# Performance work log

Hardware: AMD Instinct MI355X
Metric: run time of the kernel (lower is better)

The kernel has to match this reference:

```python
import jax, jax.numpy as jnp
import numpy as np

NS, NV = 16, 4          # scalar / vector multiplicities
MODES = 2               # spectral conv retained fourier modes
C_OUT = 40              # out irreps dim: 16 + 4*3 + 4*3
EPS = 1e-5


def setup_inputs() -> dict:
    key = jax.random.key(0)
    ks = jax.random.split(key, 10)
    T, N, E = 8, 10000, 32768
    x = jax.random.normal(ks[0], (T, N, 28), jnp.float32)
    edge_index = jax.random.randint(ks[1], (2, E), 0, N)
    edge_attr = jax.random.normal(ks[2], (T, E, 48), jnp.float32)
    edge_sh = jax.random.normal(ks[3], (T, E, 4), jnp.float32)
    s = 1.0 / np.sqrt(48.0)
    w_mlp1 = jax.random.normal(ks[4], (48, 48), jnp.float32) * s
    b_mlp1 = jnp.zeros((48,), jnp.float32)
    w_mlp2 = jax.random.normal(ks[5], (48, 416), jnp.float32) * s
    b_mlp2 = jnp.zeros((416,), jnp.float32)
    sc = 1.0 / (NS * NS)
    tc_wr = jax.random.uniform(ks[6], (NS, NS, MODES), jnp.float32) * sc
    tc_wi = jax.random.uniform(ks[7], (NS, NS, MODES), jnp.float32) * sc
    bn_gamma = jnp.ones((C_OUT,), jnp.float32)
    bn_beta = jnp.zeros((C_OUT,), jnp.float32)
    return dict(x=x, edge_index=edge_index, edge_attr=edge_attr, edge_sh=edge_sh,
                w_mlp1=w_mlp1, b_mlp1=b_mlp1, w_mlp2=w_mlp2, b_mlp2=b_mlp2,
                tc_wr=tc_wr, tc_wi=tc_wi, bn_gamma=bn_gamma, bn_beta=bn_beta)


def reference(x, edge_index, edge_attr, edge_sh,
              w_mlp1, b_mlp1, w_mlp2, b_mlp2,
              tc_wr, tc_wi, bn_gamma, bn_beta):
    T, N, _ = x.shape
    E = edge_index.shape[1]
    src, dst = edge_index[0], edge_index[1]

    # ---- SpectralConv1d over the time axis (scalar channels only) ----
    xs = x[:, :, :NS]                                   # [T,N,16]
    xf = jnp.fft.rfft(xs, axis=0)                       # [T//2+1,N,16] c64
    w = tc_wr + 1j * tc_wi                              # [16,16,M]
    low = jnp.einsum('tni,iom->tno', xf[:MODES], jnp.moveaxis(w, -1, 0).transpose(1, 2, 0)[..., :MODES]) if False else jnp.einsum('mni,iom->mno', xf[:MODES], w)
    out_ft = jnp.zeros((T // 2 + 1, N, NS), jnp.complex64).at[:MODES].set(low)
    x_scalar = jnp.fft.irfft(out_ft, n=T, axis=0)       # [T,N,16]

    # ---- edge MLP -> per-edge tensor-product weights [T,E,416] ----
    h = jax.nn.relu(edge_attr @ w_mlp1 + b_mlp1)
    ew = h @ w_mlp2 + b_mlp2

    # ---- gather source node features per edge ----
    xe = x[:, src]                                      # [T,E,28]
    s = xe[..., :NS]                                    # [T,E,16]
    v = xe[..., NS:].reshape(T, E, NV, 3)               # [T,E,4,3]
    sh0 = edge_sh[..., :1]                              # [T,E,1]
    sh1 = edge_sh[..., 1:4]                             # [T,E,3]

    # path weight splits: 0e*0e->0e | 0e*1o->1o | 1o*0e->1o | 1o*1o->0e | 1o*1o->1e
    w00 = ew[..., 0:256].reshape(T, E, NS, NS)
    w01 = ew[..., 256:320].reshape(T, E, NS, NV)
    w10 = ew[..., 320:336].reshape(T, E, NV, NV)
    w110 = ew[..., 336:400].reshape(T, E, NV, NS)
    w111 = ew[..., 400:416].reshape(T, E, NV, NV)

    inv3 = 1.0 / np.sqrt(3.0)
    inv6 = 1.0 / np.sqrt(6.0)
    n0 = 1.0 / np.sqrt(20.0)   # fan-in norm for 0e output (16 + 4 paths)
    n1o = 1.0 / np.sqrt(20.0)  # fan-in norm for 1o output (16 + 4 paths)
    n1e = 1.0 / np.sqrt(4.0)   # fan-in norm for 1e output

    # scalar outputs
    p1 = jnp.einsum('tei,teio->teo', s * sh0, w00)
    vdots = jnp.einsum('teid,ted->tei', v, sh1) * inv3
    p4 = jnp.einsum('tei,teio->teo', vdots, w110)
    out0 = (p1 + p4) * n0                               # [T,E,16]

    # odd-vector outputs
    p2 = jnp.einsum('tei,teio->teo', s, w01)[..., None] * sh1[:, :, None, :] * inv3
    p3 = jnp.einsum('teid,teio->teod', v * sh0[..., None], w10) * inv3
    out1o = (p2 + p3) * n1o                             # [T,E,4,3]

    c = jnp.cross(v, sh1[:, :, None, :]) * inv6
    out1e = jnp.einsum('teid,teio->teod', c, w111) * n1e  # [T,E,4,3]

    msg = jnp.concatenate([out0,
                           out1o.reshape(T, E, NV * 3),
                           out1e.reshape(T, E, NV * 3)], axis=-1)  # [T,E,40]

    # ---- scatter_mean over destination nodes ----
    seg = jax.vmap(lambda m: jax.ops.segment_sum(m, dst, num_segments=N))(msg)
    cnt = jax.ops.segment_sum(jnp.ones((E,), msg.dtype), dst, num_segments=N)
    y = seg / jnp.maximum(cnt, 1.0)[None, :, None]      # [T,N,40]

    # ---- add spectral time-conv result to scalar channels ----
    y = jnp.concatenate([y[..., :NS] + x_scalar, y[..., NS:]], axis=-1)

    # ---- BatchNorm1d replicating torch permute/reshape semantics ----
    z = jnp.transpose(y, (1, 2, 0)).reshape(-1, C_OUT)  # [N*T, 40] (torch layout)
    mu = z.mean(axis=0)
    var = z.var(axis=0)
    z = (z - mu) / jnp.sqrt(var + EPS) * bn_gamma + bn_beta
    y = jnp.transpose(z.reshape(N, C_OUT, T), (2, 0, 1))
    return y
```

## Files before the change

### kernel.cpp

```cpp
#include <hip/hip_runtime.h>
#include <math.h>

#define TT 8
#define NN 10000
#define EE 32768
#define CC 40
#define EPSV 1e-05f

constexpr float INV3 = 0.57735026918962576f;
constexpr float INV6 = 0.40824829046386302f;
constexpr float N0F  = 0.22360679774997896f;
constexpr float N1OF = 0.22360679774997896f;
constexpr float N1EF = 0.5f;

constexpr float CTab[8] = {1.f, 0.70710678118654752f, 0.f, -0.70710678118654752f,
                           -1.f, -0.70710678118654752f, 0.f, 0.70710678118654752f};
constexpr float STab[8] = {0.f, 0.70710678118654752f, 1.f, 0.70710678118654752f,
                           0.f, -0.70710678118654752f, -1.f, -0.70710678118654752f};

typedef __attribute__((ext_vector_type(8))) short short8;
typedef __attribute__((ext_vector_type(4))) float f32x4;

__device__ __forceinline__ void atomAdd(float* p, float v) {
  __hip_atomic_fetch_add(p, v, __ATOMIC_RELAXED, __HIP_MEMORY_SCOPE_AGENT);
}

__device__ __forceinline__ short f2bfs(float f) {
  unsigned u = __builtin_bit_cast(unsigned, f);
  u = (u + 0x7fffu + ((u >> 16) & 1u)) >> 16;
  return (short)u;
}
__device__ __forceinline__ float bf2f(ushort u) {
  unsigned v = ((unsigned)u) << 16;
  return __builtin_bit_cast(float, v);
}

#define SPEC_B 157
#define DEG_B  128
#define PREP_B 116
__global__ __launch_bounds__(256) void k_pre(const float* __restrict__ x,
                                             const float* __restrict__ wr,
                                             const float* __restrict__ wi,
                                             const int* __restrict__ ei,
                                             const float* __restrict__ W1,
                                             const float* __restrict__ W2,
                                             float* __restrict__ xsc,
                                             int* __restrict__ deg,
                                             short* __restrict__ W1F,
                                             short* __restrict__ W2F) {
  int b = blockIdx.x, tid = threadIdx.x;
  if (b < SPEC_B) {
    int gid = b * 256 + tid;
    int n = gid >> 2, og = gid & 3;
    if (n >= NN) return;
    float F0[16], A[16], B[16];
#pragma unroll
    for (int i = 0; i < 16; ++i) { F0[i] = 0.f; A[i] = 0.f; B[i] = 0.f; }
#pragma unroll
    for (int t = 0; t < 8; ++t) {
      const float4* xp = (const float4*)(x + ((size_t)t * NN + n) * 28);
      float4 v0 = xp[0], v1 = xp[1], v2 = xp[2], v3 = xp[3];
      const float ct = CTab[t], st = STab[t];
      float vv[16] = {v0.x, v0.y, v0.z, v0.w, v1.x, v1.y, v1.z, v1.w,
                      v2.x, v2.y, v2.z, v2.w, v3.x, v3.y, v3.z, v3.w};
#pragma unroll
      for (int i = 0; i < 16; ++i) {
        F0[i] += vv[i];
        A[i] = fmaf(vv[i], ct, A[i]);
        B[i] = fmaf(vv[i], -st, B[i]);
      }
    }
#pragma unroll
    for (int oo = 0; oo < 4; ++oo) {
      int o = og * 4 + oo;
      float r0 = 0.f, r1 = 0.f, i1 = 0.f;
#pragma unroll
      for (int i = 0; i < 16; ++i) {
        float wr0 = wr[i * 32 + o * 2 + 0];
        float wr1 = wr[i * 32 + o * 2 + 1];
        float wi1 = wi[i * 32 + o * 2 + 1];
        r0 = fmaf(F0[i], wr0, r0);
        r1 += A[i] * wr1 - B[i] * wi1;
        i1 += A[i] * wi1 + B[i] * wr1;
      }
#pragma unroll
      for (int t = 0; t < 8; ++t) {
        float val = 0.125f * (r0 + 2.f * (r1 * CTab[t] - i1 * STab[t]));
        xsc[((size_t)t * NN + n) * 16 + o] = val;
      }
    }
  } else if (b < SPEC_B + DEG_B) {
    int e = (b - SPEC_B) * 256 + tid;
    if (e < EE) atomicAdd(&deg[ei[EE + e]], 1);
  } else {
    int idx = (b - SPEC_B - DEG_B) * 256 + tid;
    const int tot1 = 3 * 2 * 64 * 8;
    if (idx < tot1) {
      int elem = idx & 7, lane = (idx >> 3) & 63, kt = (idx >> 9) & 1, nt = idx >> 10;
      int j = kt * 32 + ((lane >> 4) << 2) + (elem & 3) + ((elem >> 2) << 4);
      int n = nt * 16 + (lane & 15);
      W1F[idx] = (j < 48) ? f2bfs(W1[j * 48 + n]) : (short)0;
    } else {
      int id2 = idx - tot1;
      int elem = id2 & 7, lane = (id2 >> 3) & 63, kt = (id2 >> 9) & 1, ck = id2 >> 10;
      int j = kt * 32 + ((lane >> 4) << 2) + (elem & 3) + ((elem >> 2) << 4);
      int n = ck * 16 + (lane & 15);
      W2F[id2] = (j < 48) ? f2bfs(W2[j * 416 + n]) : (short)0;
    }
  }
}

__global__ __launch_bounds__(1024) void k_scan(const int* __restrict__ deg,
                                               int* __restrict__ row_start,
                                               int* __restrict__ cursor,
                                               float* __restrict__ stats) {
  __shared__ int sums[1024];
  int tid = threadIdx.x;
  if (tid < 80) stats[tid] = 0.f;
  const int PER = 10;
  int base = tid * PER;
  int s = 0;
#pragma unroll
  for (int i = 0; i < PER; ++i) {
    int idx = base + i;
    if (idx < NN) s += deg[idx];
  }
  sums[tid] = s;
  __syncthreads();
  for (int off = 1; off < 1024; off <<= 1) {
    int add = (tid >= off) ? sums[tid - off] : 0;
    __syncthreads();
    sums[tid] += add;
    __syncthreads();
  }
  int run = sums[tid] - s;
#pragma unroll
  for (int i = 0; i < PER; ++i) {
    int idx = base + i;
    if (idx < NN) {
      row_start[idx] = run;
      cursor[idx] = run;
      run += deg[idx];
    }
  }
  if (tid == 1023) row_start[NN] = run;
}

__global__ __launch_bounds__(256) void k_bucket(const int* __restrict__ ei,
                                                int* __restrict__ cursor,
                                                int* __restrict__ ipos) {
  int e = blockIdx.x * 256 + threadIdx.x;
  if (e >= EE) return;
  int d = ei[EE + e];
  int slot = atomicAdd(&cursor[d], 1);
  ipos[e] = slot;
}

__global__ __launch_bounds__(256, 4) void k_edge4(
    const float* __restrict__ x,
    const int* __restrict__ ei,
    const float* __restrict__ eag,
    const float* __restrict__ shg,
    const short* __restrict__ W1F,
    const short* __restrict__ W2F,
    const float* __restrict__ b1,
    const float* __restrict__ b2,
    const int* __restrict__ ipos,
    ushort* __restrict__ msg)
{
  __shared__ float cSs[16][64];
  __shared__ float rawSs[16][64];
  __shared__ float cVDs[4][64];
  __shared__ float vS0s[12][64];
  __shared__ float sh1fs[3][64];
  __shared__ float cCRs[12][64];
  __shared__ int   iposs[64];
  __shared__ ushort Hs[4][16][64];

  int blk = blockIdx.x;
  int t = blk >> 9;
  int e0 = (blk & 511) * 64;
  int tid = threadIdx.x;

  {
    int e = tid & 63;
    int role = tid >> 6;
    int eg = e0 + e;
    const float* shp = shg + ((size_t)t * EE + eg) * 4;
    float sh0 = shp[0], s1x = shp[1], s1y = shp[2], s1z = shp[3];
    int src = ei[eg];
    const float* xr = x + ((size_t)t * NN + src) * 28;
    const float F1 = INV3 * N1OF;
    if (role == 0) {
      iposs[e] = ipos[eg];
      sh1fs[0][e] = s1x * F1; sh1fs[1][e] = s1y * F1; sh1fs[2][e] = s1z * F1;
#pragma unroll
      for (int i = 0; i < 8; ++i) {
        float s = xr[i];
        rawSs[i][e] = s;
        cSs[i][e] = s * sh0 * N0F;
      }
    } else if (role == 1) {
#pragma unroll
      for (int i = 8; i < 16; ++i) {
        float s = xr[i];
        rawSs[i][e] = s;
        cSs[i][e] = s * sh0 * N0F;
      }
    } else {
      int i0 = (role == 2) ? 0 : 2;
#pragma unroll
      for (int ii = 0; ii < 2; ++ii) {
        int i = i0 + ii;
        float vx = xr[16 + 3 * i], vy = xr[17 + 3 * i], vz = xr[18 + 3 * i];
        cVDs[i][e] = (vx * s1x + vy * s1y + vz * s1z) * INV3 * N0F;
        vS0s[3 * i + 0][e] = vx * sh0 * F1;
        vS0s[3 * i + 1][e] = vy * sh0 * F1;
        vS0s[3 * i + 2][e] = vz * sh0 * F1;
        cCRs[3 * i + 0][e] = (vy * s1z - vz * s1y) * INV6 * N1EF;
        cCRs[3 * i + 1][e] = (vz * s1x - vx * s1z) * INV6 * N1EF;
        cCRs[3 * i + 2][e] = (vx * s1y - vy * s1x) * INV6 * N1EF;
      }
    }
  }
  __syncthreads();

  int w = tid >> 6, l = tid & 63;
  int col = l & 15;
  int kq  = (l >> 4) << 2;
  int eb  = w * 16;

  const float* row = eag + ((size_t)t * EE + e0 + eb + col) * 48;
  float4 fa = *(const float4*)(row + kq);
  float4 fb = *(const float4*)(row + 16 + kq);
  float4 fc = *(const float4*)(row + 32 + kq);
  short8 a0, a1;
  a0[0] = f2bfs(fa.x); a0[1] = f2bfs(fa.y); a0[2] = f2bfs(fa.z); a0[3] = f2bfs(fa.w);
  a0[4] = f2bfs(fb.x); a0[5] = f2bfs(fb.y); a0[6] = f2bfs(fb.z); a0[7] = f2bfs(fb.w);
  a1[0] = f2bfs(fc.x); a1[1] = f2bfs(fc.y); a1[2] = f2bfs(fc.z); a1[3] = f2bfs(fc.w);
  a1[4] = 0; a1[5] = 0; a1[6] = 0; a1[7] = 0;

  const short8* w1f = (const short8*)W1F;
  const short8* w2f = (const short8*)W2F;

#pragma unroll
  for (int nt = 0; nt < 3; ++nt) {
    float bias = b1[nt * 16 + col];
    f32x4 c = {bias, bias, bias, bias};
    c = __builtin_amdgcn_mfma_f32_16x16x32_bf16(a0, w1f[(nt * 2 + 0) * 64 + l], c, 0, 0, 0);
    c = __builtin_amdgcn_mfma_f32_16x16x32_bf16(a1, w1f[(nt * 2 + 1) * 64 + l], c, 0, 0, 0);
#pragma unroll
    for (int r = 0; r < 4; ++r) {
      int m = kq + r;
      float hv = fmaxf(c[r], 0.f);
      Hs[w][m][(nt * 16 + col) ^ ((m & 7) << 3)] = (ushort)f2bfs(hv);
    }
  }
#pragma unroll
  for (int r = 0; r < 4; ++r) {
    int m = kq + r;
    Hs[w][m][(48 + col) ^ ((m & 7) << 3)] = 0;
  }

  int m2 = col, X = (m2 & 7) << 3;
  ushort4 r0 = *(const ushort4*)&Hs[w][m2][(kq +  0) ^ X];
  ushort4 r1 = *(const ushort4*)&Hs[w][m2][(kq + 16) ^ X];
  ushort4 r2 = *(const ushort4*)&Hs[w][m2][(kq + 32) ^ X];
  ushort4 r3 = *(const ushort4*)&Hs[w][m2][(kq + 48) ^ X];
  short8 A20, A21;
  A20[0] = (short)r0.x; A20[1] = (short)r0.y; A20[2] = (short)r0.z; A20[3] = (short)r0.w;
  A20[4] = (short)r1.x; A20[5] = (short)r1.y; A20[6] = (short)r1.z; A20[7] = (short)r1.w;
  A21[0] = (short)r2.x; A21[1] = (short)r2.y; A21[2] = (short)r2.z; A21[3] = (short)r2.w;
  A21[4] = (short)r3.x; A21[5] = (short)r3.y; A21[6] = (short)r3.z; A21[7] = (short)r3.w;

  float acc0[4]  = {0.f, 0.f, 0.f, 0.f};
  float accP2[4] = {0.f, 0.f, 0.f, 0.f};
  float acc1o[3][4] = {{0.f,0.f,0.f,0.f},{0.f,0.f,0.f,0.f},{0.f,0.f,0.f,0.f}};
  float acc1e[3][4] = {{0.f,0.f,0.f,0.f},{0.f,0.f,0.f,0.f},{0.f,0.f,0.f,0.f}};
  int er0 = eb + kq;
  int iloc = col >> 2;
  int o = col & 3;

  short8 pf0[4], pf1[4];
#pragma unroll
  for (int i = 0; i < 4; ++i) {
    pf0[i] = w2f[(2 * i + 0) * 64 + l];
    pf1[i] = w2f[(2 * i + 1) * 64 + l];
  }

#pragma unroll
  for (int ck = 0; ck < 26; ++ck) {
    short8 B0 = pf0[ck & 3], B1 = pf1[ck & 3];
    if (ck + 4 < 26) {
      pf0[ck & 3] = w2f[(2 * (ck + 4) + 0) * 64 + l];
      pf1[ck & 3] = w2f[(2 * (ck + 4) + 1) * 64 + l];
    }
    float bias = b2[ck * 16 + col];
    f32x4 c = {bias, bias, bias, bias};
    c = __builtin_amdgcn_mfma_f32_16x16x32_bf16(A20, B0, c, 0, 0, 0);
    c = __builtin_amdgcn_mfma_f32_16x16x32_bf16(A21, B1, c, 0, 0, 0);

    if (ck < 16) {
#pragma unroll
      for (int r = 0; r < 4; ++r)
        acc0[r] = fmaf(cSs[ck][er0 + r], c[r], acc0[r]);
    } else if (ck < 20) {
#pragma unroll
      for (int r = 0; r < 4; ++r) {
        float q = rawSs[(ck - 16) * 4 + iloc][er0 + r] * c[r];
        q += __shfl_xor(q, 4);
        q += __shfl_xor(q, 8);
        accP2[r] += q;
      }
    } else if (ck == 20) {
#pragma unroll
      for (int d = 0; d < 3; ++d)
#pragma unroll
        for (int r = 0; r < 4; ++r) {
          float q = vS0s[iloc * 3 + d][er0 + r] * c[r];
          q += __shfl_xor(q, 4);
          q += __shfl_xor(q, 8);
          acc1o[d][r] += q;
        }
    } else if (ck < 25) {
#pragma unroll
      for (int r = 0; r < 4; ++r)
        acc0[r] = fmaf(cVDs[ck - 21][er0 + r], c[r], acc0[r]);
    } else {
#pragma unroll
      for (int d = 0; d < 3; ++d)
#pragma unroll
        for (int r = 0; r < 4; ++r) {
          float q = cCRs[iloc * 3 + d][er0 + r] * c[r];
          q += __shfl_xor(q, 4);
          q += __shfl_xor(q, 8);
          acc1e[d][r] += q;
        }
    }
  }

#pragma unroll
  for (int r = 0; r < 4; ++r) {
    size_t eg = (size_t)t * EE + iposs[er0 + r];
    msg[eg * 40 + col] = (ushort)f2bfs(acc0[r]);
  }
  if (col < 4) {
#pragma unroll
    for (int r = 0; r < 4; ++r) {
      int e = er0 + r;
      size_t eg = (size_t)t * EE + iposs[e];
      ushort* mrow = msg + eg * 40;
#pragma unroll
      for (int d = 0; d < 3; ++d) {
        mrow[16 + 3 * o + d] = (ushort)f2bfs(fmaf(accP2[r], sh1fs[d][e], acc1o[d][r]));
        mrow[28 + 3 * o + d] = (ushort)f2bfs(acc1e[d][r]);
      }
    }
  }
}

__global__ __launch_bounds__(320) void k_gstats(const ushort* __restrict__ msg,
                                                const int* __restrict__ row_start,
                                                const float* __restrict__ xsc,
                                                float* __restrict__ out,
                                                float* __restrict__ stats) {
  int blk = blockIdx.x;
  int t = blk / 157;
  int nb = blk - t * 157;
  int tid = threadIdx.x;
  int g = tid / 40, c = tid - g * 40;
  int r5 = c % 5;
  __shared__ float sred[10];
  if (tid < 10) sred[tid] = 0.f;
  __syncthreads();
  float p = 0.f, q = 0.f;
  for (int step = 0; step < 8; ++step) {
    int n = nb * 64 + step * 8 + g;
    if (n < NN) {
      int a = row_start[n], b = row_start[n + 1];
      float acc = 0.f;
      for (int j = a; j < b; ++j)
        acc += bf2f(msg[((size_t)t * EE + j) * 40 + c]);
      float y = acc / fmaxf((float)(b - a), 1.f) +
                (c < 16 ? xsc[((size_t)t * NN + n) * 16 + c] : 0.f);
      out[((size_t)t * NN + n) * 40 + c] = y;
      p += y;
      q = fmaf(y, y, q);
    }
  }
  atomicAdd(&sred[r5], p);
  atomicAdd(&sred[5 + r5], q);
  __syncthreads();
  if (tid < 10) {
    int r = tid % 5;
    int j = 8 * r + t;
    atomAdd(stats + (tid >= 5 ? 40 + j : j), sred[tid]);
  }
}

__global__ __launch_bounds__(256) void k_norm(const float* __restrict__ stats,
                                              const float* __restrict__ gam,
                                              const float* __restrict__ bet,
                                              float* __restrict__ out) {
  int idx4 = blockIdx.x * 256 + threadIdx.x;
  if (idx4 >= TT * NN * 10) return;
  int t = idx4 / (NN * 10);
  int rem = idx4 - t * NN * 10;
  int c0 = (rem % 10) * 4;
  const float inv = 1.f / (8.f * (float)NN);
  float4* op = (float4*)out;
  float4 y = op[idx4];
  float vals[4] = {y.x, y.y, y.z, y.w};
#pragma unroll
  for (int k = 0; k < 4; ++k) {
    int c = c0 + k;
    int j = 8 * (c % 5) + t;
    float mu = stats[j] * inv;
    float var = stats[40 + j] * inv - mu * mu;
    vals[k] = (vals[k] - mu) * rsqrtf(var + EPSV) * gam[j] + bet[j];
  }
  y.x = vals[0]; y.y = vals[1]; y.z = vals[2]; y.w = vals[3];
  op[idx4] = y;
}

extern "C" void kernel_launch(void* const* d_in, const int* in_sizes, int n_in,
                              void* d_out, int out_size, void* d_ws, size_t ws_size,
                              hipStream_t stream) {
  const float* x   = (const float*)d_in[0];
  const int*   ei  = (const int*)d_in[1];
  const float* ea  = (const float*)d_in[2];
  const float* esh = (const float*)d_in[3];
  const float* W1  = (const float*)d_in[4];
  const float* b1  = (const float*)d_in[5];
  const float* W2  = (const float*)d_in[6];
  const float* b2  = (const float*)d_in[7];
  const float* wr  = (const float*)d_in[8];
  const float* wi  = (const float*)d_in[9];
  const float* gam = (const float*)d_in[10];
  const float* bet = (const float*)d_in[11];
  float* out = (float*)d_out;

  float*  xsc       = (float*)d_ws;
  ushort* W1F       = (ushort*)(xsc + 1280000);
  ushort* W2F       = W1F + 3072;
  ushort* msg       = W2F + 26624;
  float*  stats     = (float*)(msg + (size_t)10485760);
  int*    deg       = (int*)(stats + 80);
  int*    cursor    = deg + 10000;
  int*    row_start = cursor + 10000;
  int*    ipos      = row_start + 10001;

  hipMemsetAsync(deg, 0, 10000 * sizeof(int), stream);

  k_pre<<<SPEC_B + DEG_B + PREP_B, 256, 0, stream>>>(x, wr, wi, ei, W1, W2, xsc, deg,
                                                     (short*)W1F, (short*)W2F);
  k_scan<<<1, 1024, 0, stream>>>(deg, row_start, cursor, stats);
  k_bucket<<<EE / 256, 256, 0, stream>>>(ei, cursor, ipos);
  k_edge4<<<TT * (EE / 64), 256, 0, stream>>>(x, ei, ea, esh, (short*)W1F, (short*)W2F,
                                              b1, b2, ipos, msg);
  k_gstats<<<TT * 157, 320, 0, stream>>>(msg, row_start, xsc, out, stats);
  k_norm<<<(TT * NN * 10 + 255) / 256, 256, 0, stream>>>(stats, gam, bet, out);
}
```

Baseline: 149.3 us.

## Fuse degree count, scan and bucketing into one single-block LDS kernel

```diff
diff --git a/kernel.cpp b/kernel.cpp
--- a/kernel.cpp
+++ b/kernel.cpp
@@ -36,16 +36,13 @@
 }
 
 #define SPEC_B 157
-#define DEG_B  128
 #define PREP_B 116
 __global__ __launch_bounds__(256) void k_pre(const float* __restrict__ x,
                                              const float* __restrict__ wr,
                                              const float* __restrict__ wi,
-                                             const int* __restrict__ ei,
                                              const float* __restrict__ W1,
                                              const float* __restrict__ W2,
                                              float* __restrict__ xsc,
-                                             int* __restrict__ deg,
                                              short* __restrict__ W1F,
                                              short* __restrict__ W2F) {
   int b = blockIdx.x, tid = threadIdx.x;
@@ -89,11 +86,8 @@
         xsc[((size_t)t * NN + n) * 16 + o] = val;
       }
     }
-  } else if (b < SPEC_B + DEG_B) {
-    int e = (b - SPEC_B) * 256 + tid;
-    if (e < EE) atomicAdd(&deg[ei[EE + e]], 1);
   } else {
-    int idx = (b - SPEC_B - DEG_B) * 256 + tid;
+    int idx = (b - SPEC_B) * 256 + tid;
     const int tot1 = 3 * 2 * 64 * 8;
     if (idx < tot1) {
       int elem = idx & 7, lane = (idx >> 3) & 63, kt = (idx >> 9) & 1, nt = idx >> 10;
@@ -110,53 +104,68 @@
   }
 }
 
-__global__ __launch_bounds__(1024) void k_scan(const int* __restrict__ deg,
-                                               int* __restrict__ row_start,
-                                               int* __restrict__ cursor,
-                                               float* __restrict__ stats) {
-  __shared__ int sums[1024];
+__global__ __launch_bounds__(1024) void k_scanbucket(const int* __restrict__ ei,
+                                                     int* __restrict__ row_start,
+                                                     int* __restrict__ ipos,
+                                                     float* __restrict__ stats) {
+  __shared__ int lcnt[NN];
+  __shared__ int wtot[16];
+  __shared__ int wpre[16];
   int tid = threadIdx.x;
   if (tid < 80) stats[tid] = 0.f;
+  for (int i = tid; i < NN; i += 1024) lcnt[i] = 0;
+  __syncthreads();
+#pragma unroll
+  for (int it = 0; it < EE / 1024; ++it) {
+    int e = it * 1024 + tid;
+    atomicAdd(&lcnt[ei[EE + e]], 1);
+  }
+  __syncthreads();
   const int PER = 10;
   int base = tid * PER;
   int s = 0;
-#pragma unroll
-  for (int i = 0; i < PER; ++i) {
-    int idx = base + i;
-    if (idx < NN) s += deg[idx];
-  }
-  sums[tid] = s;
-  __syncthreads();
-  for (int off = 1; off < 1024; off <<= 1) {
-    int add = (tid >= off) ? sums[tid - off] : 0;
-    __syncthreads();
-    sums[tid] += add;
-    __syncthreads();
-  }
-  int run = sums[tid] - s;
-#pragma unroll
-  for (int i = 0; i < PER; ++i) {
-    int idx = base + i;
-    if (idx < NN) {
-      row_start[idx] = run;
-      cursor[idx] = run;
-      run += deg[idx];
-    }
-  }
-  if (tid == 1023) row_start[NN] = run;
-}
-
-__global__ __launch_bounds__(256) void k_bucket(const int* __restrict__ ei,
-                                                int* __restrict__ cursor,
-                                                int* __restrict__ ipos) {
-  int e = blockIdx.x * 256 + threadIdx.x;
-  if (e >= EE) return;
-  int d = ei[EE + e];
-  int slot = atomicAdd(&cursor[d], 1);
-  ipos[e] = slot;
-}
-
-__global__ __launch_bounds__(256, 4) void k_edge4(
+  if (base < NN) {
+#pragma unroll
+    for (int i = 0; i < PER; ++i) s += lcnt[base + i];
+  }
+  int incl = s;
+  int lane = tid & 63, wid = tid >> 6;
+#pragma unroll
+  for (int off = 1; off < 64; off <<= 1) {
+    int v = __shfl_up(incl, off);
+    if (lane >= off) incl += v;
+  }
+  if (lane == 63) wtot[wid] = incl;
+  __syncthreads();
+  if (tid == 0) {
+    int run = 0;
+#pragma unroll
+    for (int i = 0; i < 16; ++i) { wpre[i] = run; run += wtot[i]; }
+  }
+  __syncthreads();
+  int run = wpre[wid] + (incl - s);
+  if (base < NN) {
+#pragma unroll
+    for (int i = 0; i < PER; ++i) {
+      int n = base + i;
+      int d = lcnt[n];
+      row_start[n] = run;
+      lcnt[n] = run;
+      run += d;
+    }
+  }
+  if (tid == 0) row_start[NN] = EE;
+  __syncthreads();
+#pragma unroll
+  for (int it = 0; it < EE / 1024; ++it) {
+    int e = it * 1024 + tid;
+    int d = ei[EE + e];
+    int slot = atomicAdd(&lcnt[d], 1);
+    ipos[e] = slot;
+  }
+}
+
+__global__ __launch_bounds__(256) void k_edge4(
     const float* __restrict__ x,
     const int* __restrict__ ei,
     const float* __restrict__ eag,
@@ -445,17 +454,12 @@
   ushort* W2F       = W1F + 3072;
   ushort* msg       = W2F + 26624;
   float*  stats     = (float*)(msg + (size_t)10485760);
-  int*    deg       = (int*)(stats + 80);
-  int*    cursor    = deg + 10000;
-  int*    row_start = cursor + 10000;
+  int*    row_start = (int*)(stats + 80);
   int*    ipos      = row_start + 10001;
 
-  hipMemsetAsync(deg, 0, 10000 * sizeof(int), stream);
-
-  k_pre<<<SPEC_B + DEG_B + PREP_B, 256, 0, stream>>>(x, wr, wi, ei, W1, W2, xsc, deg,
-                                                     (short*)W1F, (short*)W2F);
-  k_scan<<<1, 1024, 0, stream>>>(deg, row_start, cursor, stats);
-  k_bucket<<<EE / 256, 256, 0, stream>>>(ei, cursor, ipos);
+  k_pre<<<SPEC_B + PREP_B, 256, 0, stream>>>(x, wr, wi, W1, W2, xsc,
+                                             (short*)W1F, (short*)W2F);
+  k_scanbucket<<<1, 1024, 0, stream>>>(ei, row_start, ipos, stats);
   k_edge4<<<TT * (EE / 64), 256, 0, stream>>>(x, ei, ea, esh, (short*)W1F, (short*)W2F,
                                               b1, b2, ipos, msg);
   k_gstats<<<TT * 157, 320, 0, stream>>>(msg, row_start, xsc, out, stats);
```

Result: faster. 146.4 us (-2.0%).
